# Performance work log

Measured on AMD Instinct MI355X. Metric: run time of the kernel, lower is better.

## Reference

```python
import jax, jax.numpy as jnp
import numpy as np

B, G, DIN, DOUT = 4096, 16, 512, 512

def setup_inputs() -> dict:
    key = jax.random.key(0)
    kx, kw, kb = jax.random.split(key, 3)
    x = jax.random.normal(kx, (B, G, DIN), dtype=jnp.float32)
    # per-group nn.Linear weight: [G, dim_out, dim_in] (torch layout)
    W = jax.random.normal(kw, (G, DOUT, DIN), dtype=jnp.float32) * (1.0 / np.sqrt(DIN))
    b = jax.random.normal(kb, (G, DOUT), dtype=jnp.float32) * 0.01
    return {"x": x, "W": W, "b": b}

def reference(x, W, b):
    # MultiLinear: independent Linear per group g; y[..., g, :] = x[..., g, :] @ W[g].T + b[g]
    # Fused as a single batched GEMM over the group dimension.
    y = jnp.einsum('bgi,goi->bgo', x, W)  # [B, G, DOUT]
    return y + b
```

## Files before the change

kernel.cpp:

```cpp
#include <hip/hip_runtime.h>
#include <hip/hip_bf16.h>


#define BATCH 4096
#define NGRP  16
#define DIN   512
#define DOUT  512

#define BM 256
#define BN 256
#define BK 64
#define NT (DIN / BK)
#define LDK 72

typedef __bf16 bf16x8 __attribute__((ext_vector_type(8)));
typedef float  f32x4  __attribute__((ext_vector_type(4)));

__global__ __launch_bounds__(512, 2)
void MultiLinear_48498770706571_kernel(const float* __restrict__ X,
                                       const float* __restrict__ Wt,
                                       const float* __restrict__ Bias,
                                       float* __restrict__ Y) {
    const int bid = (blockIdx.x & 7) * 64 + (blockIdx.x >> 3);
    const int g   = bid >> 5;
    const int mt  = (bid >> 1) & 15;
    const int nt  = bid & 1;
    const int bm0 = mt * BM;
    const int bn0 = nt * BN;

    __shared__ __bf16 As[2][BM][LDK];
    __shared__ __bf16 Bs[2][BN][LDK];

    const int tid  = threadIdx.x;
    const int lane = tid & 63;
    const int w    = tid >> 6;
    const int wm   = (w >> 2) * 128;
    const int wn   = (w & 3) * 64;

    const int srow = tid >> 2;
    const int scol = (tid & 3) * 16;

    const float* pA = X + (size_t)(bm0 + srow) * (NGRP * DIN) + g * DIN + scol;
    const float* pB = Wt + (size_t)g * (DOUT * DIN) + (size_t)(bn0 + srow) * DIN + scol;
    const size_t strideA = (size_t)128 * (NGRP * DIN);
    const size_t strideB = (size_t)128 * DIN;

    f32x4 ra[2][4], rb[2][4];

#define ISSUE_LOADS(k0)                                                    \
    do {                                                                   \
        const f32x4* qa0 = (const f32x4*)(pA + (k0));                      \
        const f32x4* qa1 = (const f32x4*)(pA + strideA + (k0));            \
        const f32x4* qb0 = (const f32x4*)(pB + (k0));                      \
        const f32x4* qb1 = (const f32x4*)(pB + strideB + (k0));            \
        ra[0][0] = qa0[0]; ra[0][1] = qa0[1]; ra[0][2] = qa0[2]; ra[0][3] = qa0[3]; \
        ra[1][0] = qa1[0]; ra[1][1] = qa1[1]; ra[1][2] = qa1[2]; ra[1][3] = qa1[3]; \
        rb[0][0] = qb0[0]; rb[0][1] = qb0[1]; rb[0][2] = qb0[2]; rb[0][3] = qb0[3]; \
        rb[1][0] = qb1[0]; rb[1][1] = qb1[1]; rb[1][2] = qb1[2]; rb[1][3] = qb1[3]; \
    } while (0)

#define CVT_WRITE(buf)                                                     \
    do {                                                                   \
        _Pragma("unroll")                                                  \
        for (int p = 0; p < 2; ++p) {                                      \
            bf16x8 v0, v1, u0, u1;                                         \
            _Pragma("unroll")                                              \
            for (int j = 0; j < 4; ++j) {                                  \
                v0[j] = (__bf16)ra[p][0][j]; v0[j + 4] = (__bf16)ra[p][1][j]; \
                v1[j] = (__bf16)ra[p][2][j]; v1[j + 4] = (__bf16)ra[p][3][j]; \
                u0[j] = (__bf16)rb[p][0][j]; u0[j + 4] = (__bf16)rb[p][1][j]; \
                u1[j] = (__bf16)rb[p][2][j]; u1[j + 4] = (__bf16)rb[p][3][j]; \
            }                                                              \
            const int row = p * 128 + srow;                                \
            *(bf16x8*)&As[buf][row][scol]     = v0;                        \
            *(bf16x8*)&As[buf][row][scol + 8] = v1;                        \
            *(bf16x8*)&Bs[buf][row][scol]     = u0;                        \
            *(bf16x8*)&Bs[buf][row][scol + 8] = u1;                        \
        }                                                                  \
    } while (0)

    f32x4 acc[8][4];
#pragma unroll
    for (int mi = 0; mi < 8; ++mi)
#pragma unroll
        for (int ni = 0; ni < 4; ++ni) acc[mi][ni] = f32x4{0.f, 0.f, 0.f, 0.f};

    ISSUE_LOADS(0);
    CVT_WRITE(0);

    for (int kt = 0; kt < NT; ++kt) {
        if (kt + 1 < NT) ISSUE_LOADS((kt + 1) * BK);
        asm volatile("s_waitcnt lgkmcnt(0)" ::: "memory");
        __builtin_amdgcn_s_barrier();

        const int cur = kt & 1;
#pragma unroll
        for (int kk = 0; kk < BK; kk += 32) {
            const int ko = kk + (lane >> 4) * 8;
            bf16x8 af[8], bfr[4];
#pragma unroll
            for (int mi = 0; mi < 8; ++mi)
                af[mi] = *(const bf16x8*)&As[cur][wm + mi * 16 + (lane & 15)][ko];
#pragma unroll
            for (int ni = 0; ni < 4; ++ni)
                bfr[ni] = *(const bf16x8*)&Bs[cur][wn + ni * 16 + (lane & 15)][ko];
#pragma unroll
            for (int mi = 0; mi < 8; ++mi)
#pragma unroll
                for (int ni = 0; ni < 4; ++ni)
                    acc[mi][ni] = __builtin_amdgcn_mfma_f32_16x16x32_bf16(
                        af[mi], bfr[ni], acc[mi][ni], 0, 0, 0);
        }
        if (kt + 1 < NT) CVT_WRITE((kt + 1) & 1);
    }

    const int r0 = (lane >> 4) * 4;
    const int c  = lane & 15;
    float bias_n[4];
#pragma unroll
    for (int ni = 0; ni < 4; ++ni)
        bias_n[ni] = Bias[g * DOUT + bn0 + wn + ni * 16 + c];
#pragma unroll
    for (int mi = 0; mi < 8; ++mi) {
#pragma unroll
        for (int j = 0; j < 4; ++j) {
            const int row = bm0 + wm + mi * 16 + r0 + j;
            float* yrow = Y + (size_t)row * (NGRP * DOUT) + g * DOUT + bn0 + wn;
#pragma unroll
            for (int ni = 0; ni < 4; ++ni)
                yrow[ni * 16 + c] = acc[mi][ni][j] + bias_n[ni];
        }
    }
#undef ISSUE_LOADS
#undef CVT_WRITE
}

extern "C" void kernel_launch(void* const* d_in, const int* in_sizes, int n_in,
                              void* d_out, int out_size, void* d_ws, size_t ws_size,
                              hipStream_t stream) {
    const float* X    = (const float*)d_in[0];
    const float* Wt   = (const float*)d_in[1];
    const float* Bias = (const float*)d_in[2];
    float* Y          = (float*)d_out;

    const int grid = NGRP * (BATCH / BM) * (DOUT / BN);
    MultiLinear_48498770706571_kernel<<<grid, 512, 0, stream>>>(X, Wt, Bias, Y);
}
```

Before: 90.53 us.

## Split K-tile loop into four phases interleaving loads, LDS writes and MFMA

Each BK iteration is broken into four sub-phases, each computing half the M tile for one 32-wide K slice. The A and B global loads and their bf16 LDS writes are spread across these phases so memory traffic overlaps MFMA work. Barriers separate the phases, and s_setprio raises wave priority around the MFMA blocks. This lowers peak register pressure for fragments but adds several barriers per iteration and re-reads the B fragments.

```diff
diff --git a/kernel.cpp b/kernel.cpp
--- a/kernel.cpp
+++ b/kernel.cpp
@@ -36,6 +36,8 @@
     const int w    = tid >> 6;
     const int wm   = (w >> 2) * 128;
     const int wn   = (w & 3) * 64;
+    const int l15  = lane & 15;
+    const int kq   = (lane >> 4) * 8;
 
     const int srow = tid >> 2;
     const int scol = (tid & 3) * 16;
@@ -47,71 +49,143 @@
 
     f32x4 ra[2][4], rb[2][4];
 
-#define ISSUE_LOADS(k0)                                                    \
+#define ISSUE_A(k0)                                                        \
     do {                                                                   \
         const f32x4* qa0 = (const f32x4*)(pA + (k0));                      \
         const f32x4* qa1 = (const f32x4*)(pA + strideA + (k0));            \
+        ra[0][0] = qa0[0]; ra[0][1] = qa0[1]; ra[0][2] = qa0[2]; ra[0][3] = qa0[3]; \
+        ra[1][0] = qa1[0]; ra[1][1] = qa1[1]; ra[1][2] = qa1[2]; ra[1][3] = qa1[3]; \
+    } while (0)
+
+#define ISSUE_B(k0)                                                        \
+    do {                                                                   \
         const f32x4* qb0 = (const f32x4*)(pB + (k0));                      \
         const f32x4* qb1 = (const f32x4*)(pB + strideB + (k0));            \
-        ra[0][0] = qa0[0]; ra[0][1] = qa0[1]; ra[0][2] = qa0[2]; ra[0][3] = qa0[3]; \
-        ra[1][0] = qa1[0]; ra[1][1] = qa1[1]; ra[1][2] = qa1[2]; ra[1][3] = qa1[3]; \
         rb[0][0] = qb0[0]; rb[0][1] = qb0[1]; rb[0][2] = qb0[2]; rb[0][3] = qb0[3]; \
         rb[1][0] = qb1[0]; rb[1][1] = qb1[1]; rb[1][2] = qb1[2]; rb[1][3] = qb1[3]; \
     } while (0)
 
-#define CVT_WRITE(buf)                                                     \
+#define CVT_WRITE_A(buf)                                                   \
     do {                                                                   \
         _Pragma("unroll")                                                  \
         for (int p = 0; p < 2; ++p) {                                      \
-            bf16x8 v0, v1, u0, u1;                                         \
+            bf16x8 v0, v1;                                                 \
             _Pragma("unroll")                                              \
             for (int j = 0; j < 4; ++j) {                                  \
                 v0[j] = (__bf16)ra[p][0][j]; v0[j + 4] = (__bf16)ra[p][1][j]; \
                 v1[j] = (__bf16)ra[p][2][j]; v1[j + 4] = (__bf16)ra[p][3][j]; \
+            }                                                              \
+            *(bf16x8*)&As[buf][p * 128 + srow][scol]     = v0;             \
+            *(bf16x8*)&As[buf][p * 128 + srow][scol + 8] = v1;             \
+        }                                                                  \
+    } while (0)
+
+#define CVT_WRITE_B(buf)                                                   \
+    do {                                                                   \
+        _Pragma("unroll")                                                  \
+        for (int p = 0; p < 2; ++p) {                                      \
+            bf16x8 u0, u1;                                                 \
+            _Pragma("unroll")                                              \
+            for (int j = 0; j < 4; ++j) {                                  \
                 u0[j] = (__bf16)rb[p][0][j]; u0[j + 4] = (__bf16)rb[p][1][j]; \
                 u1[j] = (__bf16)rb[p][2][j]; u1[j + 4] = (__bf16)rb[p][3][j]; \
             }                                                              \
-            const int row = p * 128 + srow;                                \
-            *(bf16x8*)&As[buf][row][scol]     = v0;                        \
-            *(bf16x8*)&As[buf][row][scol + 8] = v1;                        \
-            *(bf16x8*)&Bs[buf][row][scol]     = u0;                        \
-            *(bf16x8*)&Bs[buf][row][scol + 8] = u1;                        \
+            *(bf16x8*)&Bs[buf][p * 128 + srow][scol]     = u0;             \
+            *(bf16x8*)&Bs[buf][p * 128 + srow][scol + 8] = u1;             \
         }                                                                  \
     } while (0)
 
+#define PHASE_BAR()                                                        \
+    do {                                                                   \
+        asm volatile("s_waitcnt lgkmcnt(0)" ::: "memory");                 \
+        __builtin_amdgcn_s_barrier();                                      \
+    } while (0)
+
     f32x4 acc[8][4];
 #pragma unroll
     for (int mi = 0; mi < 8; ++mi)
 #pragma unroll
         for (int ni = 0; ni < 4; ++ni) acc[mi][ni] = f32x4{0.f, 0.f, 0.f, 0.f};
 
-    ISSUE_LOADS(0);
-    CVT_WRITE(0);
+    ISSUE_A(0);
+    ISSUE_B(0);
+    CVT_WRITE_A(0);
+    CVT_WRITE_B(0);
+    PHASE_BAR();
 
     for (int kt = 0; kt < NT; ++kt) {
-        if (kt + 1 < NT) ISSUE_LOADS((kt + 1) * BK);
-        asm volatile("s_waitcnt lgkmcnt(0)" ::: "memory");
-        __builtin_amdgcn_s_barrier();
-
         const int cur = kt & 1;
-#pragma unroll
-        for (int kk = 0; kk < BK; kk += 32) {
-            const int ko = kk + (lane >> 4) * 8;
-            bf16x8 af[8], bfr[4];
-#pragma unroll
-            for (int mi = 0; mi < 8; ++mi)
-                af[mi] = *(const bf16x8*)&As[cur][wm + mi * 16 + (lane & 15)][ko];
-#pragma unroll
-            for (int ni = 0; ni < 4; ++ni)
-                bfr[ni] = *(const bf16x8*)&Bs[cur][wn + ni * 16 + (lane & 15)][ko];
-#pragma unroll
-            for (int mi = 0; mi < 8; ++mi)
-#pragma unroll
-                for (int ni = 0; ni < 4; ++ni)
-                    acc[mi][ni] = __builtin_amdgcn_mfma_f32_16x16x32_bf16(
-                        af[mi], bfr[ni], acc[mi][ni], 0, 0, 0);
-        }
-        if (kt + 1 < NT) CVT_WRITE((kt + 1) & 1);
+        const int nxt = cur ^ 1;
+        const bool pre = (kt + 1 < NT);
+        const int k0n = (kt + 1) * BK;
+
+        bf16x8 af[4], bfr[4];
+
+#pragma unroll
+        for (int mi = 0; mi < 4; ++mi)
+            af[mi] = *(const bf16x8*)&As[cur][wm + mi * 16 + l15][kq];
+#pragma unroll
+        for (int ni = 0; ni < 4; ++ni)
+            bfr[ni] = *(const bf16x8*)&Bs[cur][wn + ni * 16 + l15][kq];
+        if (pre) ISSUE_A(k0n);
+        PHASE_BAR();
+        __builtin_amdgcn_s_setprio(1);
+#pragma unroll
+        for (int mi = 0; mi < 4; ++mi)
+#pragma unroll
+            for (int ni = 0; ni < 4; ++ni)
+                acc[mi][ni] = __builtin_amdgcn_mfma_f32_16x16x32_bf16(
+                    af[mi], bfr[ni], acc[mi][ni], 0, 0, 0);
+        __builtin_amdgcn_s_setprio(0);
+        __builtin_amdgcn_s_barrier();
+
+#pragma unroll
+        for (int mi = 0; mi < 4; ++mi)
+            af[mi] = *(const bf16x8*)&As[cur][wm + 64 + mi * 16 + l15][kq];
+        if (pre) ISSUE_B(k0n);
+        PHASE_BAR();
+        __builtin_amdgcn_s_setprio(1);
+#pragma unroll
+        for (int mi = 0; mi < 4; ++mi)
+#pragma unroll
+            for (int ni = 0; ni < 4; ++ni)
+                acc[4 + mi][ni] = __builtin_amdgcn_mfma_f32_16x16x32_bf16(
+                    af[mi], bfr[ni], acc[4 + mi][ni], 0, 0, 0);
+        __builtin_amdgcn_s_setprio(0);
+        __builtin_amdgcn_s_barrier();
+
+#pragma unroll
+        for (int mi = 0; mi < 4; ++mi)
+            af[mi] = *(const bf16x8*)&As[cur][wm + mi * 16 + l15][32 + kq];
+#pragma unroll
+        for (int ni = 0; ni < 4; ++ni)
+            bfr[ni] = *(const bf16x8*)&Bs[cur][wn + ni * 16 + l15][32 + kq];
+        if (pre) CVT_WRITE_A(nxt);
+        PHASE_BAR();
+        __builtin_amdgcn_s_setprio(1);
+#pragma unroll
+        for (int mi = 0; mi < 4; ++mi)
+#pragma unroll
+            for (int ni = 0; ni < 4; ++ni)
+                acc[mi][ni] = __builtin_amdgcn_mfma_f32_16x16x32_bf16(
+                    af[mi], bfr[ni], acc[mi][ni], 0, 0, 0);
+        __builtin_amdgcn_s_setprio(0);
+        __builtin_amdgcn_s_barrier();
+
+#pragma unroll
+        for (int mi = 0; mi < 4; ++mi)
+            af[mi] = *(const bf16x8*)&As[cur][wm + 64 + mi * 16 + l15][32 + kq];
+        if (pre) CVT_WRITE_B(nxt);
+        PHASE_BAR();
+        __builtin_amdgcn_s_setprio(1);
+#pragma unroll
+        for (int mi = 0; mi < 4; ++mi)
+#pragma unroll
+            for (int ni = 0; ni < 4; ++ni)
+                acc[4 + mi][ni] = __builtin_amdgcn_mfma_f32_16x16x32_bf16(
+                    af[mi], bfr[ni], acc[4 + mi][ni], 0, 0, 0);
+        __builtin_amdgcn_s_setprio(0);
+        __builtin_amdgcn_s_barrier();
     }
 
     const int r0 = (lane >> 4) * 4;
@@ -131,8 +205,11 @@
                 yrow[ni * 16 + c] = acc[mi][ni][j] + bias_n[ni];
         }
     }
-#undef ISSUE_LOADS
-#undef CVT_WRITE
+#undef ISSUE_A
+#undef ISSUE_B
+#undef CVT_WRITE_A
+#undef CVT_WRITE_B
+#undef PHASE_BAR
 }
 
 extern "C" void kernel_launch(void* const* d_in, const int* in_sizes, int n_in,
```

Measured after the change: 97.89 us. +8.1%, slower.

## Pre-convert weights to bf16 and stream them into LDS via direct global-to-LDS loads

Applied to the files above, without the earlier changes.

A separate kernel converts W to bf16 in the workspace on every call. The GEMM kernel then loads B tiles straight into a swizzled flat LDS buffer with global_load_lds, so the B path no longer goes through registers or a conversion step. The main loop is unrolled by two, with separate even and odd register sets for A, to keep A prefetch and the B DMA overlapped with MFMA work. The cost is an extra kernel launch plus a full pass over W each call, and the manual vmcnt accounting has to stay correct.

```diff
diff --git a/kernel.cpp b/kernel.cpp
--- a/kernel.cpp
+++ b/kernel.cpp
@@ -11,14 +11,27 @@
 #define BN 256
 #define BK 64
 #define NT (DIN / BK)
-#define LDK 72
+#define LDKA 72
 
 typedef __bf16 bf16x8 __attribute__((ext_vector_type(8)));
 typedef float  f32x4  __attribute__((ext_vector_type(4)));
+typedef const __attribute__((address_space(1))) void gas_void;
+typedef __attribute__((address_space(3))) void las_void;
+
+__global__ __launch_bounds__(256)
+void wcvt_kernel(const float* __restrict__ W, __bf16* __restrict__ Wb) {
+    const int i = (blockIdx.x * 256 + threadIdx.x) * 8;
+    f32x4 a = *(const f32x4*)(W + i);
+    f32x4 b = *(const f32x4*)(W + i + 4);
+    bf16x8 v;
+#pragma unroll
+    for (int j = 0; j < 4; ++j) { v[j] = (__bf16)a[j]; v[j + 4] = (__bf16)b[j]; }
+    *(bf16x8*)(Wb + i) = v;
+}
 
 __global__ __launch_bounds__(512, 2)
 void MultiLinear_48498770706571_kernel(const float* __restrict__ X,
-                                       const float* __restrict__ Wt,
+                                       const __bf16* __restrict__ Wb,
                                        const float* __restrict__ Bias,
                                        float* __restrict__ Y) {
     const int bid = (blockIdx.x & 7) * 64 + (blockIdx.x >> 3);
@@ -28,54 +41,87 @@
     const int bm0 = mt * BM;
     const int bn0 = nt * BN;
 
-    __shared__ __bf16 As[2][BM][LDK];
-    __shared__ __bf16 Bs[2][BN][LDK];
+    __shared__ __bf16 As[2][BM][LDKA];
+    __shared__ __bf16 BsF[2][BN * BK];
 
     const int tid  = threadIdx.x;
     const int lane = tid & 63;
     const int w    = tid >> 6;
     const int wm   = (w >> 2) * 128;
     const int wn   = (w & 3) * 64;
+    const int l15  = lane & 15;
+    const int kq   = (lane >> 4) * 8;
 
     const int srow = tid >> 2;
     const int scol = (tid & 3) * 16;
+    const float* pA = X + (size_t)(bm0 + srow) * (NGRP * DIN) + g * DIN + scol;
+    const size_t strideA = (size_t)128 * (NGRP * DIN);
 
-    const float* pA = X + (size_t)(bm0 + srow) * (NGRP * DIN) + g * DIN + scol;
-    const float* pB = Wt + (size_t)g * (DOUT * DIN) + (size_t)(bn0 + srow) * DIN + scol;
-    const size_t strideA = (size_t)128 * (NGRP * DIN);
-    const size_t strideB = (size_t)128 * DIN;
+    const int drow0 = (w << 5) + (lane >> 3);
+    const int dch   = lane & 7;
+    const __bf16* wbase = Wb + (size_t)g * (DOUT * DIN) + (size_t)bn0 * DIN;
 
-    f32x4 ra[2][4], rb[2][4];
+    f32x4 raE[2][4], raO[2][4];
 
-#define ISSUE_LOADS(k0)                                                    \
+#define ISSUE_A(R, k0)                                                     \
     do {                                                                   \
         const f32x4* qa0 = (const f32x4*)(pA + (k0));                      \
         const f32x4* qa1 = (const f32x4*)(pA + strideA + (k0));            \
-        const f32x4* qb0 = (const f32x4*)(pB + (k0));                      \
-        const f32x4* qb1 = (const f32x4*)(pB + strideB + (k0));            \
-        ra[0][0] = qa0[0]; ra[0][1] = qa0[1]; ra[0][2] = qa0[2]; ra[0][3] = qa0[3]; \
-        ra[1][0] = qa1[0]; ra[1][1] = qa1[1]; ra[1][2] = qa1[2]; ra[1][3] = qa1[3]; \
-        rb[0][0] = qb0[0]; rb[0][1] = qb0[1]; rb[0][2] = qb0[2]; rb[0][3] = qb0[3]; \
-        rb[1][0] = qb1[0]; rb[1][1] = qb1[1]; rb[1][2] = qb1[2]; rb[1][3] = qb1[3]; \
+        R[0][0] = qa0[0]; R[0][1] = qa0[1]; R[0][2] = qa0[2]; R[0][3] = qa0[3]; \
+        R[1][0] = qa1[0]; R[1][1] = qa1[1]; R[1][2] = qa1[2]; R[1][3] = qa1[3]; \
     } while (0)
 
-#define CVT_WRITE(buf)                                                     \
+#define CVT_WRITE_A(R, buf)                                                \
     do {                                                                   \
         _Pragma("unroll")                                                  \
         for (int p = 0; p < 2; ++p) {                                      \
-            bf16x8 v0, v1, u0, u1;                                         \
+            bf16x8 v0, v1;                                                 \
             _Pragma("unroll")                                              \
             for (int j = 0; j < 4; ++j) {                                  \
-                v0[j] = (__bf16)ra[p][0][j]; v0[j + 4] = (__bf16)ra[p][1][j]; \
-                v1[j] = (__bf16)ra[p][2][j]; v1[j + 4] = (__bf16)ra[p][3][j]; \
-                u0[j] = (__bf16)rb[p][0][j]; u0[j + 4] = (__bf16)rb[p][1][j]; \
-                u1[j] = (__bf16)rb[p][2][j]; u1[j + 4] = (__bf16)rb[p][3][j]; \
+                v0[j] = (__bf16)R[p][0][j]; v0[j + 4] = (__bf16)R[p][1][j]; \
+                v1[j] = (__bf16)R[p][2][j]; v1[j + 4] = (__bf16)R[p][3][j]; \
             }                                                              \
-            const int row = p * 128 + srow;                                \
-            *(bf16x8*)&As[buf][row][scol]     = v0;                        \
-            *(bf16x8*)&As[buf][row][scol + 8] = v1;                        \
-            *(bf16x8*)&Bs[buf][row][scol]     = u0;                        \
-            *(bf16x8*)&Bs[buf][row][scol + 8] = u1;                        \
+            *(bf16x8*)&As[buf][p * 128 + srow][scol]     = v0;             \
+            *(bf16x8*)&As[buf][p * 128 + srow][scol + 8] = v1;             \
+        }                                                                  \
+    } while (0)
+
+#define DMA_B(kt, buf)                                                     \
+    do {                                                                   \
+        const size_t k0 = (size_t)(kt) * BK;                               \
+        _Pragma("unroll")                                                  \
+        for (int q = 0; q < 4; ++q) {                                      \
+            const int row = drow0 + (q << 3);                              \
+            const __bf16* gp = wbase + (size_t)row * DIN + k0              \
+                               + ((dch ^ (row & 7)) << 3);                 \
+            __builtin_amdgcn_global_load_lds(                              \
+                (gas_void*)gp,                                             \
+                (las_void*)&BsF[buf][(w << 11) + (q << 9)], 16, 0, 0);     \
+        }                                                                  \
+    } while (0)
+
+#define COMPUTE(buf)                                                       \
+    do {                                                                   \
+        _Pragma("unroll")                                                  \
+        for (int kk = 0; kk < 2; ++kk) {                                   \
+            const int ko = kk * 32 + kq;                                   \
+            bf16x8 af[8], bfr[4];                                          \
+            _Pragma("unroll")                                              \
+            for (int mi = 0; mi < 8; ++mi)                                 \
+                af[mi] = *(const bf16x8*)&As[buf][wm + mi * 16 + l15][ko]; \
+            _Pragma("unroll")                                              \
+            for (int ni = 0; ni < 4; ++ni) {                               \
+                const int brow = wn + ni * 16 + l15;                       \
+                const int ch = (lane >> 4) + kk * 4;                       \
+                bfr[ni] = *(const bf16x8*)&BsF[buf][brow * 64              \
+                            + ((ch ^ (brow & 7)) << 3)];                   \
+            }                                                              \
+            _Pragma("unroll")                                              \
+            for (int mi = 0; mi < 8; ++mi)                                 \
+                _Pragma("unroll")                                          \
+                for (int ni = 0; ni < 4; ++ni)                             \
+                    acc[mi][ni] = __builtin_amdgcn_mfma_f32_16x16x32_bf16( \
+                        af[mi], bfr[ni], acc[mi][ni], 0, 0, 0);            \
         }                                                                  \
     } while (0)
 
@@ -85,33 +131,30 @@
 #pragma unroll
         for (int ni = 0; ni < 4; ++ni) acc[mi][ni] = f32x4{0.f, 0.f, 0.f, 0.f};
 
-    ISSUE_LOADS(0);
-    CVT_WRITE(0);
+    ISSUE_A(raE, 0);
+    DMA_B(0, 0);
+    CVT_WRITE_A(raE, 0);
+    ISSUE_A(raO, BK);
 
-    for (int kt = 0; kt < NT; ++kt) {
-        if (kt + 1 < NT) ISSUE_LOADS((kt + 1) * BK);
+    for (int kt2 = 0; kt2 < NT; kt2 += 2) {
+        asm volatile("s_waitcnt vmcnt(8)" ::: "memory");
         asm volatile("s_waitcnt lgkmcnt(0)" ::: "memory");
         __builtin_amdgcn_s_barrier();
+        DMA_B(kt2 + 1, 1);
+        if (kt2 + 2 < NT) ISSUE_A(raE, (kt2 + 2) * BK);
+        COMPUTE(0);
+        CVT_WRITE_A(raO, 1);
 
-        const int cur = kt & 1;
-#pragma unroll
-        for (int kk = 0; kk < BK; kk += 32) {
-            const int ko = kk + (lane >> 4) * 8;
-            bf16x8 af[8], bfr[4];
-#pragma unroll
-            for (int mi = 0; mi < 8; ++mi)
-                af[mi] = *(const bf16x8*)&As[cur][wm + mi * 16 + (lane & 15)][ko];
-#pragma unroll
-            for (int ni = 0; ni < 4; ++ni)
-                bfr[ni] = *(const bf16x8*)&Bs[cur][wn + ni * 16 + (lane & 15)][ko];
-#pragma unroll
-            for (int mi = 0; mi < 8; ++mi)
-#pragma unroll
-                for (int ni = 0; ni < 4; ++ni)
-                    acc[mi][ni] = __builtin_amdgcn_mfma_f32_16x16x32_bf16(
-                        af[mi], bfr[ni], acc[mi][ni], 0, 0, 0);
-        }
-        if (kt + 1 < NT) CVT_WRITE((kt + 1) & 1);
+        if (kt2 + 3 < NT)
+            asm volatile("s_waitcnt vmcnt(8)" ::: "memory");
+        else
+            asm volatile("s_waitcnt vmcnt(0)" ::: "memory");
+        asm volatile("s_waitcnt lgkmcnt(0)" ::: "memory");
+        __builtin_amdgcn_s_barrier();
+        if (kt2 + 2 < NT) DMA_B(kt2 + 2, 0);
+        if (kt2 + 3 < NT) ISSUE_A(raO, (kt2 + 3) * BK);
+        COMPUTE(1);
+        if (kt2 + 2 < NT) CVT_WRITE_A(raE, 0);
     }
 
     const int r0 = (lane >> 4) * 4;
@@ -131,18 +174,23 @@
                 yrow[ni * 16 + c] = acc[mi][ni][j] + bias_n[ni];
         }
     }
-#undef ISSUE_LOADS
-#undef CVT_WRITE
+#undef ISSUE_A
+#undef CVT_WRITE_A
+#undef DMA_B
+#undef COMPUTE
 }
 
 extern "C" void kernel_launch(void* const* d_in, const int* in_sizes, int n_in,
                               void* d_out, int out_size, void* d_ws, size_t ws_size,
                               hipStream_t stream) {
     const float* X    = (const float*)d_in[0];
-    const float* Wt   = (const float*)d_in[1];
+    const float* W    = (const float*)d_in[1];
     const float* Bias = (const float*)d_in[2];
     float* Y          = (float*)d_out;
+    __bf16* Wb        = (__bf16*)d_ws;
+
+    wcvt_kernel<<<2048, 256, 0, stream>>>(W, Wb);
 
     const int grid = NGRP * (BATCH / BM) * (DOUT / BN);
-    MultiLinear_48498770706571_kernel<<<grid, 512, 0, stream>>>(X, Wt, Bias, Y);
+    MultiLinear_48498770706571_kernel<<<grid, 512, 0, stream>>>(X, Wb, Bias, Y);
 }
```

Measured after the change: 171.3 us. 1.89x slower.
